# Optimization experiments

Measured on AMD Instinct MI355X. Metric: run time of the kernel, lower is better.

Reference implementation:

```python
import jax, jax.numpy as jnp
import numpy as np

L, H, D, DK, FF = 3, 8, 128, 16, 512  # layers, heads, embed, key/val dim, ffn hidden
B, N, F_IN, OUT = 32, 512, 16, 3
SCALE = 1.0 / np.sqrt(DK)


def setup_inputs() -> dict:
    key = jax.random.key(0)
    ks = jax.random.split(key, 16)
    x = jax.random.normal(ks[0], (B, N, F_IN), dtype=jnp.float32)
    m = jax.random.randint(ks[1], (B, N, N), 0, 2).astype(jnp.int32)
    # guarantee each query attends to at least itself (avoid all -inf rows)
    m = jnp.maximum(m, jnp.eye(N, dtype=jnp.int32)[None])
    def u(k, shape, fan):
        s = 1.0 / np.sqrt(fan)
        return jax.random.uniform(k, shape, jnp.float32, -s, s)
    return {
        "x": x, "mask": m,
        "We": u(ks[2], (F_IN, D), D),
        "Wq": u(ks[3], (L, H, D, DK), DK),
        "Wk": u(ks[4], (L, H, D, DK), DK),
        "Wv": u(ks[5], (L, H, D, DK), DK),
        "Wout": u(ks[6], (L, H, DK, D), D),
        "Wff1": u(ks[7], (L, D, FF), D),
        "bff1": u(ks[8], (L, FF), D),
        "Wff2": u(ks[9], (L, FF, D), FF),
        "bff2": u(ks[10], (L, D), FF),
        "Wp": u(ks[11], (D, D), D),
        "Wr": u(ks[12], (2 * D, OUT), 2 * D),
        "br": u(ks[13], (OUT,), 2 * D),
    }


def reference(x, mask, We, Wq, Wk, Wv, Wout, Wff1, bff1, Wff2, bff2, Wp, Wr, br):
    mb = mask.astype(bool)[None]  # [1,B,N,N] broadcast over heads
    h = jax.nn.relu(x @ We)  # initial embedding [B,N,D]
    for l in range(L):
        # multi-head attention with additive skip
        Q = jnp.einsum('bnd,hdk->hbnk', h, Wq[l])
        K = jnp.einsum('bnd,hdk->hbnk', h, Wk[l])
        V = jnp.einsum('bnd,hdk->hbnk', h, Wv[l])
        compat = SCALE * jnp.einsum('hbqk,hbnk->hbqn', Q, K)  # [H,B,N,N]
        compat = jnp.where(mb, compat, -jnp.inf)
        attn = jax.nn.softmax(compat, axis=-1)
        # note: torch's attn.clone()[...] = 0 is a no-op, so no re-zeroing
        heads = jnp.einsum('hbqn,hbnk->hbqk', attn, V)
        h = h + jnp.einsum('hbqk,hkd->bqd', heads, Wout[l])
        # feed-forward with additive skip
        h = h + jax.nn.relu(h @ Wff1[l] + bff1[l]) @ Wff2[l] + bff2[l] * 0 + (jax.nn.relu(h @ Wff1[l] + bff1[l]) @ Wff2[l] + bff2[l] - (jax.nn.relu(h @ Wff1[l] + bff1[l]) @ Wff2[l]))  # placeholder removed below
    return h


# clean faithful version (used)
def reference(x, mask, We, Wq, Wk, Wv, Wout, Wff1, bff1, Wff2, bff2, Wp, Wr, br):
    mb = mask.astype(bool)[None]  # [1,B,N,N]
    h = jax.nn.relu(x @ We)  # [B,N,D]
    for l in range(L):
        Q = jnp.einsum('bnd,hdk->hbnk', h, Wq[l])
        K = jnp.einsum('bnd,hdk->hbnk', h, Wk[l])
        V = jnp.einsum('bnd,hdk->hbnk', h, Wv[l])
        compat = SCALE * jnp.einsum('hbqk,hbnk->hbqn', Q, K)
        compat = jnp.where(mb, compat, -jnp.inf)
        attn = jax.nn.softmax(compat, axis=-1)
        heads = jnp.einsum('hbqn,hbnk->hbqk', attn, V)
        h = h + jnp.einsum('hbqk,hkd->bqd', heads, Wout[l])
        h = h + (jax.nn.relu(h @ Wff1[l] + bff1[l]) @ Wff2[l] + bff2[l])
    # readout (actor head: output_dim=3)
    h_pooled = (h.mean(axis=1)) @ Wp  # [B,D]
    f_pooled = jnp.broadcast_to(h_pooled[:, None, :], h.shape)  # [B,N,D]
    features = jax.nn.relu(jnp.concatenate([f_pooled, h], axis=-1))  # [B,N,2D]
    return features @ Wr + br  # [B,N,3]
```

## Files before the change

### kernel.cpp

```cpp
#include <hip/hip_runtime.h>
#include <cstdint>
#include <cstddef>

#define L_LAYERS 3
#define H_HEADS 8
#define D_EMB 128
#define DKV 16
#define FF_DIM 512
#define B_BATCH 32
#define N_SEQ 512
#define F_INP 16
#define OUT_DIM 3
#define M_ROWS (B_BATCH * N_SEQ)
#define QSCALE 0.3606737602222409f

typedef unsigned short ushort_t;
typedef unsigned int uint_t;
typedef __attribute__((ext_vector_type(8))) short short8;
typedef __attribute__((ext_vector_type(4))) float f32x4;
typedef __attribute__((ext_vector_type(16))) float f32x16;

__device__ inline ushort_t f2bf(float x) {
    union { float f; uint_t u; } v; v.f = x;
    uint_t r = v.u + 0x7fffu + ((v.u >> 16) & 1u);
    return (ushort_t)(r >> 16);
}

__device__ inline uint_t pack2bf_tr(float a, float b) {
    union { float f; uint_t u; } ua, ub;
    ua.f = a; ub.f = b;
    return (ua.u >> 16) | (ub.u & 0xffff0000u);
}

__device__ inline float exp2fast(float x) {
#if __has_builtin(__builtin_amdgcn_exp2f)
    return __builtin_amdgcn_exp2f(x);
#else
    float r; __asm__("v_exp_f32 %0, %1" : "=v"(r) : "v"(x)); return r;
#endif
}

__device__ inline void gload16(const void* g, void* l) {
    __builtin_amdgcn_global_load_lds(
        (const __attribute__((address_space(1))) unsigned int*)g,
        (__attribute__((address_space(3))) unsigned int*)l, 16, 0, 0);
}

#define PM_BLK 32768
#define RQ_BLK 576
#define TW_BLK 192
#define T1_BLK 768
#define T2_BLK 768
#define PB_BLK 16
#define EM_BLK 8192
__global__ __launch_bounds__(256) void preproc_kernel(
        const int* __restrict__ mask, unsigned long long* __restrict__ pm,
        const float* __restrict__ Wq, const float* __restrict__ Wk,
        const float* __restrict__ Wv, ushort_t* __restrict__ wqkvT,
        const float* __restrict__ Wout, ushort_t* __restrict__ woutT,
        const float* __restrict__ Wff1, ushort_t* __restrict__ wff1T,
        const float* __restrict__ Wff2, ushort_t* __restrict__ wff2T,
        float* __restrict__ pbsum,
        const float* __restrict__ x, const float* __restrict__ We,
        float* __restrict__ hf, ushort_t* __restrict__ hb) {
    int bx = blockIdx.x;
    const int tid = threadIdx.x;
    if (bx < PM_BLK) {
        int gid = bx * 256 + tid;
        int v = mask[gid];
        unsigned long long bal = __ballot(v != 0);
        if ((tid & 63) == 0) pm[gid >> 6] = bal;
        return;
    }
    bx -= PM_BLK;
    if (bx < RQ_BLK) {
        int idx = bx * 256 + tid;
        int d = idx & 127;
        int n = (idx >> 7) % 384;
        int l = idx / (384 * 128);
        int proj = n >> 7, hh = (n & 127) >> 4, kk = n & 15;
        const float* src = proj == 0 ? Wq : proj == 1 ? Wk : Wv;
        wqkvT[idx] = f2bf(src[((size_t)(l * 8 + hh) * 128 + d) * 16 + kk]);
        return;
    }
    bx -= RQ_BLK;
    if (bx < TW_BLK + T1_BLK + T2_BLK) {
        const float* src; ushort_t* dst; int R, C;
        if (bx < TW_BLK) { src = Wout; dst = woutT; R = 128; C = 128; }
        else if (bx < TW_BLK + T1_BLK) { src = Wff1; dst = wff1T; R = 128; C = 512; bx -= TW_BLK; }
        else { src = Wff2; dst = wff2T; R = 512; C = 128; bx -= TW_BLK + T1_BLK; }
        int idx = bx * 256 + tid;
        int b = idx / (R * C);
        int rem = idx - b * (R * C);
        int r = rem / C, c = rem - r * C;
        dst[(size_t)b * R * C + (size_t)c * R + r] = f2bf(src[idx]);
        return;
    }
    bx -= TW_BLK + T1_BLK + T2_BLK;
    if (bx < PB_BLK) {
        pbsum[bx * 256 + tid] = 0.f;
        return;
    }
    bx -= PB_BLK;
    {
        const int d = tid & 127;
        const int m = bx * 2 + (tid >> 7);
        const float* xr = x + (size_t)m * 16;
        float acc = 0.f;
#pragma unroll
        for (int k = 0; k < 16; k++) acc += xr[k] * We[k * 128 + d];
        acc = fmaxf(acc, 0.f);
        hf[(size_t)m * 128 + d] = acc;
        hb[(size_t)m * 128 + d] = f2bf(acc);
    }
}

__global__ __launch_bounds__(512, 2) void qkv_attn_kernel(
        const ushort_t* __restrict__ hb,
        const ushort_t* __restrict__ WqkvT,
        const uint_t* __restrict__ pm,
        ushort_t* __restrict__ Aout) {
    __shared__ __align__(16) ushort_t sm[26752];
    ushort_t* KF = sm;
    ushort_t* Vt = sm + 8192;
    ushort_t* Qs = sm + 16512;
    ushort_t* Ws = sm + 20608;
    ushort_t* Ps = sm + 16512;

    const int tid = threadIdx.x;
    const int w = tid >> 6, L = tid & 63;
    const int lr = L & 15, lq = L >> 4;
    const int lane31 = L & 31, lhalf = L >> 5;
    const int bx = blockIdx.x;
    const int b = bx >> 4, h = (bx >> 1) & 7, half = bx & 1;

    for (int i = tid; i < 768; i += 512) {
        const int row = i >> 4, cg = i & 15;
        const int proj = row >> 4, kk = row & 15;
        gload16(WqkvT + (size_t)(proj * 128 + h * 16 + kk) * 128 + cg * 8, &Ws[i * 8]);
    }
    __syncthreads();

    const ushort_t* Ab = hb + (size_t)b * 512 * 128;
    for (int mc = 0; mc < 4; mc++) {
        f32x4 acc[3];
#pragma unroll
        for (int j = 0; j < 3; j++) acc[j] = (f32x4){0.f, 0.f, 0.f, 0.f};
#pragma unroll
        for (int k0 = 0; k0 < 128; k0 += 32) {
            short8 af = *(const short8*)(Ab + (size_t)(mc * 128 + w * 16 + lr) * 128 + k0 + lq * 8);
#pragma unroll
            for (int j = 0; j < 3; j++) {
                short8 bf = *(const short8*)&Ws[(j * 16 + lr) * 128 + k0 + lq * 8];
                acc[j] = __builtin_amdgcn_mfma_f32_16x16x32_bf16(af, bf, acc[j], 0, 0, 0);
            }
        }
        const int rbase = mc * 128 + w * 16 + lq * 4;
#pragma unroll
        for (int r = 0; r < 4; r++) {
            const int key = rbase + r;
            KF[(key >> 5) * 512 + ((lr >> 3) * 32 + (key & 31)) * 8 + (lr & 7)] = f2bf(acc[1][r]);
            Vt[lr * 520 + key] = f2bf(acc[2][r]);
        }
        if ((mc >> 1) == half) {
            const int qb = (mc & 1) * 128 + w * 16 + lq * 4;
#pragma unroll
            for (int r = 0; r < 4; r++)
                Qs[(qb + r) * 16 + lr] = f2bf(acc[0][r] * QSCALE);
        }
    }
    __syncthreads();

    const int q0g = half * 256 + w * 32;
    const short8 qf = *(const short8*)&Qs[(w * 32 + lane31) * 16 + lhalf * 8];
    const uint_t* pmr = pm + (size_t)(b * 512 + q0g + lane31) * 16;
    const uint4 mwa = *(const uint4*)(pmr);
    const uint4 mwb = *(const uint4*)(pmr + 4);
    const uint4 mwc = *(const uint4*)(pmr + 8);
    const uint4 mwd = *(const uint4*)(pmr + 12);
    const uint_t mw[16] = {mwa.x, mwa.y, mwa.z, mwa.w, mwb.x, mwb.y, mwb.z, mwb.w,
                           mwc.x, mwc.y, mwc.z, mwc.w, mwd.x, mwd.y, mwd.z, mwd.w};
    __syncthreads();

    const f32x16 zero16 = (f32x16)(0.f);
    short8 vone;
#pragma unroll
    for (int i = 0; i < 8; i++) vone[i] = (short)0x3F80;

    f32x4 oacc0 = (f32x4){0.f, 0.f, 0.f, 0.f};
    f32x4 oacc1 = (f32x4){0.f, 0.f, 0.f, 0.f};
    f32x4 lacc0 = (f32x4){0.f, 0.f, 0.f, 0.f};
    f32x4 lacc1 = (f32x4){0.f, 0.f, 0.f, 0.f};
#pragma unroll
    for (int t = 0; t < 16; t++) {
        short8 kf = *(const short8*)&KF[t * 512 + L * 8];
        f32x16 s = __builtin_amdgcn_mfma_f32_32x32x16_bf16(kf, qf, zero16, 0, 0, 0);
        const uint_t word = mw[t];
#pragma unroll
        for (int r = 0; r < 16; r++) {
            const int keyl = (r & 3) + 8 * (r >> 2) + 4 * lhalf;
            const float e = exp2fast(s[r]);
            s[r] = (word & (1u << keyl)) ? e : 0.f;
        }
#pragma unroll
        for (int g = 0; g < 4; g++) {
            const uint_t lo = pack2bf_tr(s[g * 4 + 0], s[g * 4 + 1]);
            const uint_t hi = pack2bf_tr(s[g * 4 + 2], s[g * 4 + 3]);
            *(uint2*)&Ps[w * 1152 + lane31 * 36 + g * 8 + 4 * lhalf] = make_uint2(lo, hi);
        }
        short8 vb = *(const short8*)&Vt[lr * 520 + t * 32 + lq * 8];
        short8 pa0 = *(const short8*)&Ps[w * 1152 + lr * 36 + lq * 8];
        short8 pa1 = *(const short8*)&Ps[w * 1152 + (16 + lr) * 36 + lq * 8];
        oacc0 = __builtin_amdgcn_mfma_f32_16x16x32_bf16(pa0, vb, oacc0, 0, 0, 0);
        oacc1 = __builtin_amdgcn_mfma_f32_16x16x32_bf16(pa1, vb, oacc1, 0, 0, 0);
        lacc0 = __builtin_amdgcn_mfma_f32_16x16x32_bf16(pa0, vone, lacc0, 0, 0, 0);
        lacc1 = __builtin_amdgcn_mfma_f32_16x16x32_bf16(pa1, vone, lacc1, 0, 0, 0);
    }

#pragma unroll
    for (int qa = 0; qa < 2; qa++) {
        const f32x4 oa = qa ? oacc1 : oacc0;
        const f32x4 la = qa ? lacc1 : lacc0;
#pragma unroll
        for (int rr = 0; rr < 4; rr++) {
            const int qloc = qa * 16 + lq * 4 + rr;
            Aout[(size_t)(b * 512 + q0g + qloc) * 128 + h * 16 + lr] = f2bf(oa[rr] / la[rr]);
        }
    }
}

__global__ __launch_bounds__(256, 2) void tail_kernel(
        const ushort_t* __restrict__ A,
        const ushort_t* __restrict__ WoT,
        const ushort_t* __restrict__ W1T,
        const ushort_t* __restrict__ W2T,
        const float* __restrict__ b1,
        const float* __restrict__ b2,
        float* __restrict__ hf, ushort_t* __restrict__ hb,
        float* __restrict__ pbsum, int accum) {
    __shared__ __align__(16) ushort_t sm[39424];
    ushort_t* AsA = sm;
    ushort_t* AsB = sm + 1024;
    ushort_t* BsA = sm + 2048;
    ushort_t* BsB = sm + 10240;
    ushort_t* C1b = sm + 18432;
    ushort_t* T   = sm + 22784;

    const int tid = threadIdx.x;
    const int w = tid >> 6, l = tid & 63;
    const int lr = l & 15, lq = l >> 4;
    const int srow = (l >> 2);
    const int scol = (l & 3) * 8;
    const int m0 = blockIdx.x * 32;

    f32x4 c1a[2][2];
#pragma unroll
    for (int i = 0; i < 2; i++)
#pragma unroll
        for (int j = 0; j < 2; j++) c1a[i][j] = (f32x4){0.f, 0.f, 0.f, 0.f};
    if (w < 2)
        gload16(A + (size_t)(m0 + w * 16 + srow) * 128 + scol, &AsA[(w * 16 + srow) * 32 + scol]);
#pragma unroll
    for (int it = 0; it < 2; it++)
        gload16(WoT + (size_t)(it * 64 + w * 16 + srow) * 128 + scol, &BsA[(it * 64 + w * 16 + srow) * 32 + scol]);
#pragma unroll
    for (int k0 = 0; k0 < 128; k0 += 32) {
        ushort_t* Ac = (k0 & 32) ? AsB : AsA;
        ushort_t* Bc = (k0 & 32) ? BsB : BsA;
        ushort_t* An = (k0 & 32) ? AsA : AsB;
        ushort_t* Bn = (k0 & 32) ? BsA : BsB;
        __syncthreads();
        if (k0 + 32 < 128) {
            if (w < 2)
                gload16(A + (size_t)(m0 + w * 16 + srow) * 128 + k0 + 32 + scol,
                        &An[(w * 16 + srow) * 32 + scol]);
#pragma unroll
            for (int it = 0; it < 2; it++)
                gload16(WoT + (size_t)(it * 64 + w * 16 + srow) * 128 + k0 + 32 + scol,
                        &Bn[(it * 64 + w * 16 + srow) * 32 + scol]);
        }
        short8 af[2], bfr[2];
#pragma unroll
        for (int i = 0; i < 2; i++) af[i] = *(const short8*)&Ac[(i * 16 + lr) * 32 + lq * 8];
#pragma unroll
        for (int j = 0; j < 2; j++) bfr[j] = *(const short8*)&Bc[(w * 32 + j * 16 + lr) * 32 + lq * 8];
#pragma unroll
        for (int i = 0; i < 2; i++)
#pragma unroll
            for (int j = 0; j < 2; j++)
                c1a[i][j] = __builtin_amdgcn_mfma_f32_16x16x32_bf16(af[i], bfr[j], c1a[i][j], 0, 0, 0);
    }
    float c1[2][2][4];
#pragma unroll
    for (int i = 0; i < 2; i++)
#pragma unroll
        for (int r = 0; r < 4; r++) {
            const int row = i * 16 + lq * 4 + r;
#pragma unroll
            for (int j = 0; j < 2; j++) {
                const int n = w * 32 + j * 16 + lr;
                const float v = c1a[i][j][r] + hf[(size_t)(m0 + row) * 128 + n];
                c1[i][j][r] = v;
                C1b[row * 136 + n] = f2bf(v);
            }
        }

#pragma unroll
    for (int it = 0; it < 4; it++)
        gload16(W1T + (size_t)(it * 64 + w * 16 + srow) * 128 + scol, &BsA[(it * 64 + w * 16 + srow) * 32 + scol]);
#pragma unroll
    for (int nc = 0; nc < 2; nc++) {
        f32x4 ta[2][4];
#pragma unroll
        for (int i = 0; i < 2; i++)
#pragma unroll
            for (int j = 0; j < 4; j++) ta[i][j] = (f32x4){0.f, 0.f, 0.f, 0.f};
#pragma unroll
        for (int k0i = 0; k0i < 4; k0i++) {
            const int c = nc * 4 + k0i;
            ushort_t* Bc = (c & 1) ? BsB : BsA;
            ushort_t* Bn = (c & 1) ? BsA : BsB;
            __syncthreads();
            if (c + 1 < 8) {
                const int nc2 = (c + 1) >> 2, k02 = ((c + 1) & 3) * 32;
#pragma unroll
                for (int it = 0; it < 4; it++)
                    gload16(W1T + (size_t)(nc2 * 256 + it * 64 + w * 16 + srow) * 128 + k02 + scol,
                            &Bn[(it * 64 + w * 16 + srow) * 32 + scol]);
            }
            short8 af[2], bfr[4];
#pragma unroll
            for (int i = 0; i < 2; i++)
                af[i] = *(const short8*)&C1b[(i * 16 + lr) * 136 + k0i * 32 + lq * 8];
#pragma unroll
            for (int j = 0; j < 4; j++)
                bfr[j] = *(const short8*)&Bc[(w * 64 + j * 16 + lr) * 32 + lq * 8];
#pragma unroll
            for (int i = 0; i < 2; i++)
#pragma unroll
                for (int j = 0; j < 4; j++)
                    ta[i][j] = __builtin_amdgcn_mfma_f32_16x16x32_bf16(af[i], bfr[j], ta[i][j], 0, 0, 0);
        }
#pragma unroll
        for (int j = 0; j < 4; j++) {
            const int n = nc * 256 + w * 64 + j * 16 + lr;
            const float bv = b1[n];
#pragma unroll
            for (int i = 0; i < 2; i++)
#pragma unroll
                for (int r = 0; r < 4; r++) {
                    const int row = i * 16 + lq * 4 + r;
                    T[row * 520 + n] = f2bf(fmaxf(ta[i][j][r] + bv, 0.f));
                }
        }
    }

#pragma unroll
    for (int it = 0; it < 2; it++)
        gload16(W2T + (size_t)(it * 64 + w * 16 + srow) * 512 + scol, &BsA[(it * 64 + w * 16 + srow) * 32 + scol]);
    f32x4 oa[2][2];
#pragma unroll
    for (int i = 0; i < 2; i++)
#pragma unroll
        for (int j = 0; j < 2; j++) oa[i][j] = (f32x4){0.f, 0.f, 0.f, 0.f};
#pragma unroll
    for (int k0 = 0; k0 < 512; k0 += 32) {
        ushort_t* Bc = ((k0 >> 5) & 1) ? BsB : BsA;
        ushort_t* Bn = ((k0 >> 5) & 1) ? BsA : BsB;
        __syncthreads();
        if (k0 + 32 < 512) {
#pragma unroll
            for (int it = 0; it < 2; it++)
                gload16(W2T + (size_t)(it * 64 + w * 16 + srow) * 512 + k0 + 32 + scol,
                        &Bn[(it * 64 + w * 16 + srow) * 32 + scol]);
        }
        short8 af[2], bfr[2];
#pragma unroll
        for (int i = 0; i < 2; i++)
            af[i] = *(const short8*)&T[(i * 16 + lr) * 520 + k0 + lq * 8];
#pragma unroll
        for (int j = 0; j < 2; j++)
            bfr[j] = *(const short8*)&Bc[(w * 32 + j * 16 + lr) * 32 + lq * 8];
#pragma unroll
        for (int i = 0; i < 2; i++)
#pragma unroll
            for (int j = 0; j < 2; j++)
                oa[i][j] = __builtin_amdgcn_mfma_f32_16x16x32_bf16(af[i], bfr[j], oa[i][j], 0, 0, 0);
    }
#pragma unroll
    for (int j = 0; j < 2; j++) {
        const int n = w * 32 + j * 16 + lr;
        const float bv = b2[n];
        float psum = 0.f;
#pragma unroll
        for (int i = 0; i < 2; i++)
#pragma unroll
            for (int r = 0; r < 4; r++) {
                const int row = i * 16 + lq * 4 + r;
                const float v = oa[i][j][r] + bv + c1[i][j][r];
                psum += v;
                hf[(size_t)(m0 + row) * 128 + n] = v;
                hb[(size_t)(m0 + row) * 128 + n] = f2bf(v);
            }
        if (accum) {
            psum += __shfl_xor(psum, 16);
            psum += __shfl_xor(psum, 32);
            if (lq == 0) atomicAdd(&pbsum[(m0 >> 9) * 128 + n], psum);
        }
    }
}

__global__ __launch_bounds__(256) void readout_kernel(const float* __restrict__ h,
                                                      const float* __restrict__ pbsum,
                                                      const float* __restrict__ Wp,
                                                      const float* __restrict__ Wr,
                                                      const float* __restrict__ br,
                                                      float* __restrict__ out) {
    const int u = blockIdx.x;
    const int b = u >> 4;
    const int m0 = u * 32;
    const int t = threadIdx.x;
    __shared__ float pooled[128];
    __shared__ float rp[128];
    __shared__ float pb3[3];
    if (t < 128) pooled[t] = pbsum[b * 128 + t] * (1.0f / 512.0f);
    __syncthreads();
    if (t < 128) {
        float a = 0.f;
        for (int dd = 0; dd < 128; dd++) a += pooled[dd] * Wp[dd * 128 + t];
        rp[t] = fmaxf(a, 0.f);
    }
    __syncthreads();
    if (t < OUT_DIM) {
        float a = br[t];
        for (int j = 0; j < 128; j++) a += rp[j] * Wr[j * 3 + t];
        pb3[t] = a;
    }
    __syncthreads();
    const int j = t & 7;
    const int row = m0 + (t >> 3);
    const float* hr = h + (size_t)row * 128 + j * 16;
    float a0 = 0.f, a1 = 0.f, a2o = 0.f;
#pragma unroll
    for (int dd = 0; dd < 16; dd++) {
        const float v = fmaxf(hr[dd], 0.f);
        const float* wr = Wr + (size_t)(128 + j * 16 + dd) * 3;
        a0 += v * wr[0]; a1 += v * wr[1]; a2o += v * wr[2];
    }
#pragma unroll
    for (int off = 4; off; off >>= 1) {
        a0 += __shfl_down(a0, off, 8);
        a1 += __shfl_down(a1, off, 8);
        a2o += __shfl_down(a2o, off, 8);
    }
    if (j == 0) {
        out[(size_t)row * 3 + 0] = a0 + pb3[0];
        out[(size_t)row * 3 + 1] = a1 + pb3[1];
        out[(size_t)row * 3 + 2] = a2o + pb3[2];
    }
}

extern "C" void kernel_launch(void* const* d_in, const int* in_sizes, int n_in,
                              void* d_out, int out_size, void* d_ws, size_t ws_size,
                              hipStream_t stream) {
    const float* x    = (const float*)d_in[0];
    const int*   mask = (const int*)d_in[1];
    const float* We   = (const float*)d_in[2];
    const float* Wq   = (const float*)d_in[3];
    const float* Wk   = (const float*)d_in[4];
    const float* Wv   = (const float*)d_in[5];
    const float* Wout = (const float*)d_in[6];
    const float* Wff1 = (const float*)d_in[7];
    const float* bff1 = (const float*)d_in[8];
    const float* Wff2 = (const float*)d_in[9];
    const float* bff2 = (const float*)d_in[10];
    const float* Wp   = (const float*)d_in[11];
    const float* Wr   = (const float*)d_in[12];
    const float* br   = (const float*)d_in[13];
    float* out = (float*)d_out;

    char* ws = (char*)d_ws;
    unsigned long long* pm64 = (unsigned long long*)(ws + 0);
    const uint_t* pm32       = (const uint_t*)(ws + 0);
    ushort_t* wqkvT = (ushort_t*)(ws + 1048576);
    ushort_t* woutT = (ushort_t*)(ws + 1343488);
    ushort_t* wff1T = (ushort_t*)(ws + 1441792);
    ushort_t* wff2T = (ushort_t*)(ws + 1835008);
    float*    pbsum = (float*)(ws + 2228224);
    float*    hbuf  = (float*)(ws + 4194304);
    ushort_t* hb16  = (ushort_t*)(ws + 12582912);
    ushort_t* a16   = (ushort_t*)(ws + 41943040);

    preproc_kernel<<<PM_BLK + RQ_BLK + TW_BLK + T1_BLK + T2_BLK + PB_BLK + EM_BLK, 256, 0, stream>>>(
        mask, pm64, Wq, Wk, Wv, wqkvT, Wout, woutT, Wff1, wff1T, Wff2, wff2T,
        pbsum, x, We, hbuf, hb16);

    for (int l = 0; l < L_LAYERS; l++) {
        qkv_attn_kernel<<<512, 512, 0, stream>>>(
            hb16, wqkvT + (size_t)l * 384 * 128, pm32, a16);
        tail_kernel<<<M_ROWS / 32, 256, 0, stream>>>(
            a16, woutT + (size_t)l * 128 * 128, wff1T + (size_t)l * 512 * 128,
            wff2T + (size_t)l * 128 * 512, bff1 + l * 512, bff2 + l * 128,
            hbuf, hb16, pbsum, (l == L_LAYERS - 1) ? 1 : 0);
    }

    readout_kernel<<<512, 256, 0, stream>>>(hbuf, pbsum, Wp, Wr, br, out);
}
```

Before: 271.4 us.

## Software-pipeline attention loop with double-buffered P tiles and perm-based bf16 packing

The attention inner loop is restructured so the QK^T MFMA for tile t is issued alongside the PV MFMAs for tile t-1. Two shared-memory P buffers alternate so the exp/mask work of one tile can overlap matrix work of the previous one. The bf16 pair packing also switches to a single v_perm byte-permute. Shared memory per block grows from about 53KB to about 70KB, which may limit how many blocks fit on a CU at the 2-blocks launch bound.

```diff
diff --git a/kernel.cpp b/kernel.cpp
--- a/kernel.cpp
+++ b/kernel.cpp
@@ -29,7 +29,11 @@
 __device__ inline uint_t pack2bf_tr(float a, float b) {
     union { float f; uint_t u; } ua, ub;
     ua.f = a; ub.f = b;
+#if __has_builtin(__builtin_amdgcn_perm)
+    return __builtin_amdgcn_perm(ub.u, ua.u, 0x07060302u);
+#else
     return (ua.u >> 16) | (ub.u & 0xffff0000u);
+#endif
 }
 
 __device__ inline float exp2fast(float x) {
@@ -120,12 +124,13 @@
         const ushort_t* __restrict__ WqkvT,
         const uint_t* __restrict__ pm,
         ushort_t* __restrict__ Aout) {
-    __shared__ __align__(16) ushort_t sm[26752];
-    ushort_t* KF = sm;
-    ushort_t* Vt = sm + 8192;
-    ushort_t* Qs = sm + 16512;
-    ushort_t* Ws = sm + 20608;
-    ushort_t* Ps = sm + 16512;
+    __shared__ __align__(16) ushort_t sm[34944];
+    ushort_t* KF  = sm;
+    ushort_t* Vt  = sm + 8192;
+    ushort_t* Qs  = sm + 16512;
+    ushort_t* Ws  = sm + 20608;
+    ushort_t* PsA = sm + 16512;
+    ushort_t* PsB = sm + 25728;
 
     const int tid = threadIdx.x;
     const int w = tid >> 6, L = tid & 63;
@@ -191,31 +196,65 @@
     f32x4 oacc1 = (f32x4){0.f, 0.f, 0.f, 0.f};
     f32x4 lacc0 = (f32x4){0.f, 0.f, 0.f, 0.f};
     f32x4 lacc1 = (f32x4){0.f, 0.f, 0.f, 0.f};
-#pragma unroll
-    for (int t = 0; t < 16; t++) {
-        short8 kf = *(const short8*)&KF[t * 512 + L * 8];
-        f32x16 s = __builtin_amdgcn_mfma_f32_32x32x16_bf16(kf, qf, zero16, 0, 0, 0);
-        const uint_t word = mw[t];
-#pragma unroll
-        for (int r = 0; r < 16; r++) {
-            const int keyl = (r & 3) + 8 * (r >> 2) + 4 * lhalf;
-            const float e = exp2fast(s[r]);
-            s[r] = (word & (1u << keyl)) ? e : 0.f;
-        }
-#pragma unroll
-        for (int g = 0; g < 4; g++) {
-            const uint_t lo = pack2bf_tr(s[g * 4 + 0], s[g * 4 + 1]);
-            const uint_t hi = pack2bf_tr(s[g * 4 + 2], s[g * 4 + 3]);
-            *(uint2*)&Ps[w * 1152 + lane31 * 36 + g * 8 + 4 * lhalf] = make_uint2(lo, hi);
-        }
-        short8 vb = *(const short8*)&Vt[lr * 520 + t * 32 + lq * 8];
-        short8 pa0 = *(const short8*)&Ps[w * 1152 + lr * 36 + lq * 8];
-        short8 pa1 = *(const short8*)&Ps[w * 1152 + (16 + lr) * 36 + lq * 8];
-        oacc0 = __builtin_amdgcn_mfma_f32_16x16x32_bf16(pa0, vb, oacc0, 0, 0, 0);
-        oacc1 = __builtin_amdgcn_mfma_f32_16x16x32_bf16(pa1, vb, oacc1, 0, 0, 0);
-        lacc0 = __builtin_amdgcn_mfma_f32_16x16x32_bf16(pa0, vone, lacc0, 0, 0, 0);
-        lacc1 = __builtin_amdgcn_mfma_f32_16x16x32_bf16(pa1, vone, lacc1, 0, 0, 0);
-    }
+
+#define CS_STEP(T_IDX, PS) do {                                                     \
+    short8 kf = *(const short8*)&KF[(T_IDX) * 512 + L * 8];                         \
+    f32x16 s = __builtin_amdgcn_mfma_f32_32x32x16_bf16(kf, qf, zero16, 0, 0, 0);    \
+    const uint_t word = mw[(T_IDX)];                                                \
+    _Pragma("unroll")                                                               \
+    for (int r = 0; r < 16; r++) {                                                  \
+        const int keyl = (r & 3) + 8 * (r >> 2) + 4 * lhalf;                        \
+        const float e = exp2fast(s[r]);                                             \
+        s[r] = (word & (1u << keyl)) ? e : 0.f;                                     \
+    }                                                                               \
+    _Pragma("unroll")                                                               \
+    for (int g = 0; g < 4; g++) {                                                   \
+        const uint_t lo = pack2bf_tr(s[g * 4 + 0], s[g * 4 + 1]);                   \
+        const uint_t hi = pack2bf_tr(s[g * 4 + 2], s[g * 4 + 3]);                   \
+        *(uint2*)&(PS)[w * 1152 + lane31 * 36 + g * 8 + 4 * lhalf] = make_uint2(lo, hi); \
+    }                                                                               \
+} while (0)
+
+#define PV_STEP(T_IDX, PS) do {                                                     \
+    short8 vb = *(const short8*)&Vt[lr * 520 + (T_IDX) * 32 + lq * 8];              \
+    short8 pa0 = *(const short8*)&(PS)[w * 1152 + lr * 36 + lq * 8];                \
+    short8 pa1 = *(const short8*)&(PS)[w * 1152 + (16 + lr) * 36 + lq * 8];         \
+    oacc0 = __builtin_amdgcn_mfma_f32_16x16x32_bf16(pa0, vb, oacc0, 0, 0, 0);       \
+    oacc1 = __builtin_amdgcn_mfma_f32_16x16x32_bf16(pa1, vb, oacc1, 0, 0, 0);       \
+    lacc0 = __builtin_amdgcn_mfma_f32_16x16x32_bf16(pa0, vone, lacc0, 0, 0, 0);     \
+    lacc1 = __builtin_amdgcn_mfma_f32_16x16x32_bf16(pa1, vone, lacc1, 0, 0, 0);     \
+} while (0)
+
+#define PIPE_STEP(T_IDX, PSCUR, PSPREV) do {                                        \
+    short8 kf = *(const short8*)&KF[(T_IDX) * 512 + L * 8];                         \
+    f32x16 s = __builtin_amdgcn_mfma_f32_32x32x16_bf16(kf, qf, zero16, 0, 0, 0);    \
+    PV_STEP((T_IDX) - 1, PSPREV);                                                   \
+    const uint_t word = mw[(T_IDX)];                                                \
+    _Pragma("unroll")                                                               \
+    for (int r = 0; r < 16; r++) {                                                  \
+        const int keyl = (r & 3) + 8 * (r >> 2) + 4 * lhalf;                        \
+        const float e = exp2fast(s[r]);                                             \
+        s[r] = (word & (1u << keyl)) ? e : 0.f;                                     \
+    }                                                                               \
+    _Pragma("unroll")                                                               \
+    for (int g = 0; g < 4; g++) {                                                   \
+        const uint_t lo = pack2bf_tr(s[g * 4 + 0], s[g * 4 + 1]);                   \
+        const uint_t hi = pack2bf_tr(s[g * 4 + 2], s[g * 4 + 3]);                   \
+        *(uint2*)&(PSCUR)[w * 1152 + lane31 * 36 + g * 8 + 4 * lhalf] = make_uint2(lo, hi); \
+    }                                                                               \
+} while (0)
+
+    CS_STEP(0, PsA);
+#pragma unroll
+    for (int tp = 0; tp < 7; tp++) {
+        PIPE_STEP(2 * tp + 1, PsB, PsA);
+        PIPE_STEP(2 * tp + 2, PsA, PsB);
+    }
+    PIPE_STEP(15, PsB, PsA);
+    PV_STEP(15, PsB);
+#undef CS_STEP
+#undef PV_STEP
+#undef PIPE_STEP
 
 #pragma unroll
     for (int qa = 0; qa < 2; qa++) {
```

After: 267.1 us. About the same (-1.6%).

## Keep P in registers via lane swaps, fold row-sum into PV MFMA, halve attention grid

Applied to the files above, without the earlier changes.

The attention kernel now has each block handle all 512 queries of one (batch, head) pair, so K/V projection is no longer computed twice per head. The softmax probabilities stay in registers and are rearranged with cross-lane shuffles instead of being staged through LDS. The row sum is produced by padding V with a ones column and using a 32x32 MFMA, which replaces the separate l-accumulator MFMAs. The preprocessing kernel loops over more work per block and switches its weight transposes to coalesced writes. The grid is halved to 256 blocks, which may underfill the GPU, and LDS usage grows.

```diff
diff --git a/kernel.cpp b/kernel.cpp
--- a/kernel.cpp
+++ b/kernel.cpp
@@ -29,7 +29,11 @@
 __device__ inline uint_t pack2bf_tr(float a, float b) {
     union { float f; uint_t u; } ua, ub;
     ua.f = a; ub.f = b;
+#if __has_builtin(__builtin_amdgcn_perm)
+    return __builtin_amdgcn_perm(ub.u, ua.u, 0x07060302u);
+#else
     return (ua.u >> 16) | (ub.u & 0xffff0000u);
+#endif
 }
 
 __device__ inline float exp2fast(float x) {
@@ -46,13 +50,21 @@
         (__attribute__((address_space(3))) unsigned int*)l, 16, 0, 0);
 }
 
-#define PM_BLK 32768
+__device__ inline void plswap(uint_t a, uint_t b, uint_t& ra, uint_t& rb) {
+    const uint_t sb = (uint_t)__shfl_xor((int)b, 32);
+    const uint_t sa = (uint_t)__shfl_xor((int)a, 32);
+    const bool lo = (threadIdx.x & 32) == 0;
+    ra = lo ? sb : a;
+    rb = lo ? b : sa;
+}
+
+#define PM_BLK 2048
 #define RQ_BLK 576
 #define TW_BLK 192
 #define T1_BLK 768
 #define T2_BLK 768
 #define PB_BLK 16
-#define EM_BLK 8192
+#define EM_BLK 1024
 __global__ __launch_bounds__(256) void preproc_kernel(
         const int* __restrict__ mask, unsigned long long* __restrict__ pm,
         const float* __restrict__ Wq, const float* __restrict__ Wk,
@@ -66,10 +78,13 @@
     int bx = blockIdx.x;
     const int tid = threadIdx.x;
     if (bx < PM_BLK) {
-        int gid = bx * 256 + tid;
-        int v = mask[gid];
-        unsigned long long bal = __ballot(v != 0);
-        if ((tid & 63) == 0) pm[gid >> 6] = bal;
+#pragma unroll 4
+        for (int it = 0; it < 16; ++it) {
+            const int gid = (bx * 16 + it) * 256 + tid;
+            const int v = mask[gid];
+            const unsigned long long bal = __ballot(v != 0);
+            if ((tid & 63) == 0) pm[gid >> 6] = bal;
+        }
         return;
     }
     bx -= PM_BLK;
@@ -92,8 +107,8 @@
         int idx = bx * 256 + tid;
         int b = idx / (R * C);
         int rem = idx - b * (R * C);
-        int r = rem / C, c = rem - r * C;
-        dst[(size_t)b * R * C + (size_t)c * R + r] = f2bf(src[idx]);
+        int c = rem / R, r = rem - c * R;
+        dst[idx] = f2bf(src[((size_t)b * R + r) * C + c]);
         return;
     }
     bx -= TW_BLK + T1_BLK + T2_BLK;
@@ -104,41 +119,44 @@
     bx -= PB_BLK;
     {
         const int d = tid & 127;
-        const int m = bx * 2 + (tid >> 7);
-        const float* xr = x + (size_t)m * 16;
-        float acc = 0.f;
-#pragma unroll
-        for (int k = 0; k < 16; k++) acc += xr[k] * We[k * 128 + d];
-        acc = fmaxf(acc, 0.f);
-        hf[(size_t)m * 128 + d] = acc;
-        hb[(size_t)m * 128 + d] = f2bf(acc);
-    }
-}
-
-__global__ __launch_bounds__(512, 2) void qkv_attn_kernel(
+#pragma unroll 2
+        for (int it = 0; it < 8; ++it) {
+            const int m = (bx * 8 + it) * 2 + (tid >> 7);
+            const float* xr = x + (size_t)m * 16;
+            float acc = 0.f;
+#pragma unroll
+            for (int k = 0; k < 16; k++) acc += xr[k] * We[k * 128 + d];
+            acc = fmaxf(acc, 0.f);
+            hf[(size_t)m * 128 + d] = acc;
+            hb[(size_t)m * 128 + d] = f2bf(acc);
+        }
+    }
+}
+
+__global__ __launch_bounds__(512, 4) void qkv_attn_kernel(
         const ushort_t* __restrict__ hb,
         const ushort_t* __restrict__ WqkvT,
         const uint_t* __restrict__ pm,
         ushort_t* __restrict__ Aout) {
-    __shared__ __align__(16) ushort_t sm[26752];
+    __shared__ __align__(16) ushort_t sm[39168];
     ushort_t* KF = sm;
     ushort_t* Vt = sm + 8192;
-    ushort_t* Qs = sm + 16512;
-    ushort_t* Ws = sm + 20608;
-    ushort_t* Ps = sm + 16512;
+    ushort_t* Qs = sm + 24832;
+    ushort_t* Ws = sm + 33024;
 
     const int tid = threadIdx.x;
     const int w = tid >> 6, L = tid & 63;
     const int lr = L & 15, lq = L >> 4;
     const int lane31 = L & 31, lhalf = L >> 5;
     const int bx = blockIdx.x;
-    const int b = bx >> 4, h = (bx >> 1) & 7, half = bx & 1;
+    const int b = bx >> 3, h = bx & 7;
 
     for (int i = tid; i < 768; i += 512) {
         const int row = i >> 4, cg = i & 15;
         const int proj = row >> 4, kk = row & 15;
         gload16(WqkvT + (size_t)(proj * 128 + h * 16 + kk) * 128 + cg * 8, &Ws[i * 8]);
     }
+    for (int i = tid; i < 8320; i += 512) Vt[8320 + i] = (ushort_t)0x3F80;
     __syncthreads();
 
     const ushort_t* Ab = hb + (size_t)b * 512 * 128;
@@ -161,70 +179,68 @@
             const int key = rbase + r;
             KF[(key >> 5) * 512 + ((lr >> 3) * 32 + (key & 31)) * 8 + (lr & 7)] = f2bf(acc[1][r]);
             Vt[lr * 520 + key] = f2bf(acc[2][r]);
-        }
-        if ((mc >> 1) == half) {
-            const int qb = (mc & 1) * 128 + w * 16 + lq * 4;
-#pragma unroll
-            for (int r = 0; r < 4; r++)
-                Qs[(qb + r) * 16 + lr] = f2bf(acc[0][r] * QSCALE);
+            Qs[(key) * 16 + lr] = f2bf(acc[0][r] * QSCALE);
         }
     }
     __syncthreads();
 
-    const int q0g = half * 256 + w * 32;
-    const short8 qf = *(const short8*)&Qs[(w * 32 + lane31) * 16 + lhalf * 8];
-    const uint_t* pmr = pm + (size_t)(b * 512 + q0g + lane31) * 16;
-    const uint4 mwa = *(const uint4*)(pmr);
-    const uint4 mwb = *(const uint4*)(pmr + 4);
-    const uint4 mwc = *(const uint4*)(pmr + 8);
-    const uint4 mwd = *(const uint4*)(pmr + 12);
-    const uint_t mw[16] = {mwa.x, mwa.y, mwa.z, mwa.w, mwb.x, mwb.y, mwb.z, mwb.w,
-                           mwc.x, mwc.y, mwc.z, mwc.w, mwd.x, mwd.y, mwd.z, mwd.w};
-    __syncthreads();
+    const short8 qf0 = *(const short8*)&Qs[(w * 32 + lane31) * 16 + lhalf * 8];
+    const short8 qf1 = *(const short8*)&Qs[(256 + w * 32 + lane31) * 16 + lhalf * 8];
 
     const f32x16 zero16 = (f32x16)(0.f);
-    short8 vone;
-#pragma unroll
-    for (int i = 0; i < 8; i++) vone[i] = (short)0x3F80;
-
-    f32x4 oacc0 = (f32x4){0.f, 0.f, 0.f, 0.f};
-    f32x4 oacc1 = (f32x4){0.f, 0.f, 0.f, 0.f};
-    f32x4 lacc0 = (f32x4){0.f, 0.f, 0.f, 0.f};
-    f32x4 lacc1 = (f32x4){0.f, 0.f, 0.f, 0.f};
-#pragma unroll
-    for (int t = 0; t < 16; t++) {
-        short8 kf = *(const short8*)&KF[t * 512 + L * 8];
-        f32x16 s = __builtin_amdgcn_mfma_f32_32x32x16_bf16(kf, qf, zero16, 0, 0, 0);
-        const uint_t word = mw[t];
+
+    for (int qloop = 0; qloop < 2; ++qloop) {
+        const int q0g = qloop * 256 + w * 32;
+        const short8 qf = qloop ? qf1 : qf0;
+        const uint_t* pmr = pm + (size_t)(b * 512 + q0g + lane31) * 16;
+        const uint4 mwa = *(const uint4*)(pmr);
+        const uint4 mwb = *(const uint4*)(pmr + 4);
+        const uint4 mwc = *(const uint4*)(pmr + 8);
+        const uint4 mwd = *(const uint4*)(pmr + 12);
+        const uint_t mw[16] = {mwa.x, mwa.y, mwa.z, mwa.w, mwb.x, mwb.y, mwb.z, mwb.w,
+                               mwc.x, mwc.y, mwc.z, mwc.w, mwd.x, mwd.y, mwd.z, mwd.w};
+
+        f32x16 oacc = zero16;
+
+#pragma unroll
+        for (int t = 0; t < 16; ++t) {
+            short8 kf = *(const short8*)&KF[t * 512 + L * 8];
+            f32x16 s = __builtin_amdgcn_mfma_f32_32x32x16_bf16(kf, qf, zero16, 0, 0, 0);
+            const uint_t word = mw[t];
+#pragma unroll
+            for (int r = 0; r < 16; r++) {
+                const int keyl = (r & 3) + 8 * (r >> 2) + 4 * lhalf;
+                const float e = exp2fast(s[r]);
+                s[r] = (word & (1u << keyl)) ? e : 0.f;
+            }
+            uint_t u0 = pack2bf_tr(s[0], s[1]),  u1 = pack2bf_tr(s[2], s[3]);
+            uint_t u2 = pack2bf_tr(s[4], s[5]),  u3 = pack2bf_tr(s[6], s[7]);
+            uint_t u4 = pack2bf_tr(s[8], s[9]),  u5 = pack2bf_tr(s[10], s[11]);
+            uint_t u6 = pack2bf_tr(s[12], s[13]), u7 = pack2bf_tr(s[14], s[15]);
+
+            uint_t f0, f1, f2, f3;
+            plswap(u2, u0, f2, f0);
+            plswap(u3, u1, f3, f1);
+            union { uint_t u[4]; short8 s8; } cv0;
+            cv0.u[0] = f0; cv0.u[1] = f1; cv0.u[2] = f2; cv0.u[3] = f3;
+            short8 vb0 = *(const short8*)&Vt[lane31 * 520 + t * 32 + lhalf * 8];
+            oacc = __builtin_amdgcn_mfma_f32_32x32x16_bf16(cv0.s8, vb0, oacc, 0, 0, 0);
+
+            uint_t g0, g1, g2, g3;
+            plswap(u6, u4, g2, g0);
+            plswap(u7, u5, g3, g1);
+            union { uint_t u[4]; short8 s8; } cv1;
+            cv1.u[0] = g0; cv1.u[1] = g1; cv1.u[2] = g2; cv1.u[3] = g3;
+            short8 vb1 = *(const short8*)&Vt[lane31 * 520 + t * 32 + 16 + lhalf * 8];
+            oacc = __builtin_amdgcn_mfma_f32_32x32x16_bf16(cv1.s8, vb1, oacc, 0, 0, 0);
+        }
+
 #pragma unroll
         for (int r = 0; r < 16; r++) {
-            const int keyl = (r & 3) + 8 * (r >> 2) + 4 * lhalf;
-            const float e = exp2fast(s[r]);
-            s[r] = (word & (1u << keyl)) ? e : 0.f;
-        }
-#pragma unroll
-        for (int g = 0; g < 4; g++) {
-            const uint_t lo = pack2bf_tr(s[g * 4 + 0], s[g * 4 + 1]);
-            const uint_t hi = pack2bf_tr(s[g * 4 + 2], s[g * 4 + 3]);
-            *(uint2*)&Ps[w * 1152 + lane31 * 36 + g * 8 + 4 * lhalf] = make_uint2(lo, hi);
-        }
-        short8 vb = *(const short8*)&Vt[lr * 520 + t * 32 + lq * 8];
-        short8 pa0 = *(const short8*)&Ps[w * 1152 + lr * 36 + lq * 8];
-        short8 pa1 = *(const short8*)&Ps[w * 1152 + (16 + lr) * 36 + lq * 8];
-        oacc0 = __builtin_amdgcn_mfma_f32_16x16x32_bf16(pa0, vb, oacc0, 0, 0, 0);
-        oacc1 = __builtin_amdgcn_mfma_f32_16x16x32_bf16(pa1, vb, oacc1, 0, 0, 0);
-        lacc0 = __builtin_amdgcn_mfma_f32_16x16x32_bf16(pa0, vone, lacc0, 0, 0, 0);
-        lacc1 = __builtin_amdgcn_mfma_f32_16x16x32_bf16(pa1, vone, lacc1, 0, 0, 0);
-    }
-
-#pragma unroll
-    for (int qa = 0; qa < 2; qa++) {
-        const f32x4 oa = qa ? oacc1 : oacc0;
-        const f32x4 la = qa ? lacc1 : lacc0;
-#pragma unroll
-        for (int rr = 0; rr < 4; rr++) {
-            const int qloc = qa * 16 + lq * 4 + rr;
-            Aout[(size_t)(b * 512 + q0g + qloc) * 128 + h * 16 + lr] = f2bf(oa[rr] / la[rr]);
+            const int qrow = (r & 3) + 8 * (r >> 2) + 4 * lhalf;
+            const float lsum = __shfl(oacc[r], (L & 32) | 16);
+            if (lane31 < 16)
+                Aout[(size_t)(b * 512 + q0g + qrow) * 128 + h * 16 + lane31] = f2bf(oacc[r] / lsum);
         }
     }
 }
@@ -496,7 +512,7 @@
         pbsum, x, We, hbuf, hb16);
 
     for (int l = 0; l < L_LAYERS; l++) {
-        qkv_attn_kernel<<<512, 512, 0, stream>>>(
+        qkv_attn_kernel<<<256, 512, 0, stream>>>(
             hb16, wqkvT + (size_t)l * 384 * 128, pm32, a16);
         tail_kernel<<<M_ROWS / 32, 256, 0, stream>>>(
             a16, woutT + (size_t)l * 128 * 128, wff1T + (size_t)l * 512 * 128,
```

After: 362.6 us. 33.6% more time.
